# Performance work log

Hardware: AMD Instinct MI355X
Metric: run time of the kernel (lower is better)

Reference implementation:

```python
import jax, jax.numpy as jnp
import numpy as np

DIM = 384
HEADS = 6
NEG = -1e9  # masked-score fill; equivalent to gathering only kept K/V rows


def setup_inputs() -> dict:
    key = jax.random.key(0)
    ks = jax.random.split(key, 9)
    B, N, C = 1, 4098, DIM
    x = jax.random.normal(ks[0], (B, N, C), dtype=jnp.float32)
    pos = jax.random.normal(ks[1], (B, N + 1, C), dtype=jnp.float32)
    # float mask in [0,1); >=0.5 means 'foreground / keep as key', <0.5 pooled into back token
    mask = jax.random.uniform(ks[2], (B, 1, N - 2), dtype=jnp.float32)
    mask_block = jnp.ones((N + 1,), dtype=jnp.float32)  # positions 0, N-1, N always kept
    Wq = jax.random.normal(ks[3], (C, C), dtype=jnp.float32) * 0.02
    Wk = jax.random.normal(ks[4], (C, C), dtype=jnp.float32) * 0.02
    Wv = jax.random.normal(ks[5], (C, C), dtype=jnp.float32) * 0.02
    Wp = jax.random.normal(ks[6], (C, C), dtype=jnp.float32) * 0.02
    bp = jnp.zeros((C,), dtype=jnp.float32)
    return {"x": x, "pos": pos, "mask": mask, "mask_block": mask_block,
            "Wq": Wq, "Wk": Wk, "Wv": Wv, "Wp": Wp, "bp": bp}


def reference(x, pos, mask, mask_block, Wq, Wk, Wv, Wp, bp):
    B, N, C = x.shape
    H = HEADS
    D = C // H
    scale = D ** -0.5
    eps = 1e-10

    # back token: average of background (mask < 0.5) interior tokens
    reverse = jnp.where(mask < 0.5, 1.0, 0.0)                      # (B,1,N-2)
    pooled = jnp.einsum('bon,bnc->boc', reverse, x[:, 1:N - 1])    # (B,1,C)
    back_tokens = pooled / (reverse.sum(axis=2, keepdims=True) + eps)

    kv_x = jnp.concatenate([x, back_tokens], axis=1)               # (B,N+1,C)
    q_x = x + pos[:, :N]
    k_x = kv_x + pos

    q = (q_x @ Wq.T).reshape(B, N, H, D).transpose(0, 2, 1, 3)       # (B,H,N,D)
    k = (k_x @ Wk.T).reshape(B, N + 1, H, D).transpose(0, 2, 1, 3)   # (B,H,N+1,D)
    v = (kv_x @ Wv.T).reshape(B, N + 1, H, D).transpose(0, 2, 1, 3)  # (B,H,N+1,D)

    # key-selection mask: original gathers rows with mask_block >= 0.5;
    # masked softmax over all N+1 keys is mathematically identical.
    mb = mask_block.at[1:N - 1].set(mask[0, 0])
    keep = mb >= 0.5                                               # (N+1,)

    scores = jnp.einsum('bhqd,bhkd->bhqk', q, k) * scale
    scores = jnp.where(keep[None, None, None, :], scores, NEG)
    attn = jax.nn.softmax(scores, axis=-1)
    out = jnp.einsum('bhqk,bhkd->bhqd', attn, v)
    out = out.transpose(0, 2, 1, 3).reshape(B, N, C)
    return out @ Wp.T + bp
```

## Files before the change

kernel.cpp:

```cpp
#include <hip/hip_runtime.h>
#include <math.h>

#define N_TOK 4098
#define NK_TOK 4099
#define C_DIM 384
#define NKPAD 4160

typedef short  bh8 __attribute__((ext_vector_type(8)));
typedef float  f32x4 __attribute__((ext_vector_type(4)));
typedef unsigned short ushort;
typedef ushort u4 __attribute__((ext_vector_type(4)));
typedef ushort u8 __attribute__((ext_vector_type(8)));

static __device__ __forceinline__ ushort f2bf(float f) {
  unsigned int u = __float_as_uint(f);
  u = (u + 0x7FFF + ((u >> 16) & 1)) >> 16;
  return (ushort)u;
}
static __device__ __forceinline__ float bf2f(ushort s) {
  return __uint_as_float(((unsigned int)s) << 16);
}

__global__ __launch_bounds__(256) void prep_kernel(
    const float* __restrict__ x, const float* __restrict__ pos,
    const float* __restrict__ mask, const float* __restrict__ mask_block,
    const float* __restrict__ Wq, const float* __restrict__ Wk,
    const float* __restrict__ Wv, const float* __restrict__ Wp,
    float* __restrict__ pooled_part, float* __restrict__ cnt_part,
    int* __restrict__ nk, int* __restrict__ inv,
    ushort* __restrict__ Ak, ushort* __restrict__ Av, ushort* __restrict__ Wb) {
  const int b = blockIdx.x, t = threadIdx.x;
  if (b < 64) {
    __shared__ float smask[64];
    const int r0 = b * 64;
    if (t < 64) smask[t] = mask[r0 + t];
    __syncthreads();
    float a0 = 0.f, a1 = 0.f;
    int lc = 0;
#pragma unroll 8
    for (int i = 0; i < 64; ++i) {
      if (smask[i] < 0.5f) {
        a0 += x[(size_t)(r0 + i + 1) * C_DIM + t];
        if (t < 128) a1 += x[(size_t)(r0 + i + 1) * C_DIM + 256 + t];
        ++lc;
      }
    }
    pooled_part[b * C_DIM + t] = a0;
    if (t < 128) pooled_part[b * C_DIM + 256 + t] = a1;
    if (t == 0) cnt_part[b] = (float)lc;
  } else if (b == 64) {
    __shared__ int scnt[256];
    const int j0 = t * 17;
    unsigned int bits = 0;
    int c = 0;
#pragma unroll 1
    for (int u = 0; u < 17; ++u) {
      const int j = j0 + u;
      bool keep = false;
      if (j < NK_TOK)
        keep = (j >= 1 && j <= N_TOK - 2) ? (mask[j - 1] >= 0.5f)
                                          : (mask_block[j] >= 0.5f);
      if (keep) { bits |= 1u << u; ++c; }
    }
    scnt[t] = c;
    __syncthreads();
    for (int d = 1; d < 256; d <<= 1) {
      const int v = scnt[t];
      const int add = (t >= d) ? scnt[t - d] : 0;
      __syncthreads();
      scnt[t] = v + add;
      __syncthreads();
    }
    int base = scnt[t] - c;
    if (t == 255) *nk = scnt[255];
#pragma unroll 1
    for (int u = 0; u < 17; ++u) {
      const int j = j0 + u;
      if (j < NK_TOK) inv[j] = ((bits >> u) & 1) ? base++ : -1;
    }
  } else if (b < 194) {
    const int r0 = (b - 65) * 32;
#pragma unroll 3
    for (int i = 0; i < 12; ++i) {
      const int idx = i * 1024 + t * 4;
      const int row = r0 + idx / C_DIM, col = idx % C_DIM;
      if (row >= N_TOK) continue;
      const float4 pv = *(const float4*)&pos[(size_t)row * C_DIM + col];
      const float4 xv = *(const float4*)&x[(size_t)row * C_DIM + col];
      u4 k4 = {f2bf(xv.x + pv.x), f2bf(xv.y + pv.y),
               f2bf(xv.z + pv.z), f2bf(xv.w + pv.w)};
      *(u4*)&Ak[(size_t)row * C_DIM + col] = k4;
      u4 v4 = {f2bf(xv.x), f2bf(xv.y), f2bf(xv.z), f2bf(xv.w)};
      *(u4*)&Av[(size_t)row * C_DIM + col] = v4;
    }
  } else {
    const int wi = b - 194;
    const float* src = (wi < 8) ? Wq : (wi < 16) ? Wk : (wi < 24) ? Wv : Wp;
    const int base = (wi >> 3) * 147456 + (wi & 7) * 18432;
#pragma unroll 2
    for (int i = 0; i < 18; ++i) {
      const float4 v = *(const float4*)&src[(wi & 7) * 18432 + i * 1024 + t * 4];
      u4 o = {f2bf(v.x), f2bf(v.y), f2bf(v.z), f2bf(v.w)};
      *(u4*)&Wb[base + i * 1024 + t * 4] = o;
    }
  }
}

static __device__ __forceinline__ void gemm_core(
    const ushort* __restrict__ A, const ushort* __restrict__ B,
    ushort (* __restrict__ As)[72], ushort (* __restrict__ Bs)[72],
    int t, int w, int quad, int l15, f32x4 acc[4]) {
  const int g = t & 7;
  u8 ra[2], rb[2];
#pragma unroll
  for (int it = 0; it < 2; ++it) {
    const int r = it * 32 + (t >> 3);
    ra[it] = *(const u8*)&A[r * C_DIM + g * 8];
    rb[it] = *(const u8*)&B[r * C_DIM + g * 8];
  }
#pragma unroll 1
  for (int kt = 0; kt < 6; ++kt) {
    __syncthreads();
#pragma unroll
    for (int it = 0; it < 2; ++it) {
      const int r = it * 32 + (t >> 3);
      *(u8*)&As[r][g * 8] = ra[it];
      *(u8*)&Bs[r][g * 8] = rb[it];
    }
    __syncthreads();
    if (kt < 5) {
      const int k0 = (kt + 1) * 64;
#pragma unroll
      for (int it = 0; it < 2; ++it) {
        const int r = it * 32 + (t >> 3);
        ra[it] = *(const u8*)&A[r * C_DIM + k0 + g * 8];
        rb[it] = *(const u8*)&B[r * C_DIM + k0 + g * 8];
      }
    }
    const bh8 b0 = *(const bh8*)&Bs[w * 16 + l15][quad * 8];
    const bh8 b1 = *(const bh8*)&Bs[w * 16 + l15][32 + quad * 8];
#pragma unroll
    for (int mb = 0; mb < 4; ++mb) {
      const bh8 a0 = *(const bh8*)&As[mb * 16 + l15][quad * 8];
      const bh8 a1 = *(const bh8*)&As[mb * 16 + l15][32 + quad * 8];
      acc[mb] = __builtin_amdgcn_mfma_f32_16x16x32_bf16(a0, b0, acc[mb], 0, 0, 0);
      acc[mb] = __builtin_amdgcn_mfma_f32_16x16x32_bf16(a1, b1, acc[mb], 0, 0, 0);
    }
  }
}

__global__ __launch_bounds__(256) void gemm3_kernel(
    const ushort* __restrict__ Ak, const ushort* __restrict__ Av,
    const ushort* __restrict__ Wb, const int* __restrict__ inv,
    const float* __restrict__ pooled_part, const float* __restrict__ cnt_part,
    const float* __restrict__ pos, ushort* __restrict__ Qh,
    ushort* __restrict__ Kc, ushort* __restrict__ Vt) {
  __shared__ ushort As[64][72], Bs[64][72];
  __shared__ float skin[C_DIM], svin[C_DIM];
  const int t = threadIdx.x, w = t >> 6, lane = t & 63;
  const int quad = lane >> 4, l15 = lane & 15;
  const int which = blockIdx.y / 6, h = blockIdx.y % 6;

  if (blockIdx.x == 65) {
    if (blockIdx.y != 0) return;
    float cs = 0.f;
#pragma unroll 8
    for (int i = 0; i < 64; ++i) cs += cnt_part[i];
    const float ic = 1.f / (cs + 1e-10f);
    for (int c = t; c < C_DIM; c += 256) {
      float s = 0.f;
#pragma unroll 8
      for (int p = 0; p < 64; ++p) s += pooled_part[p * C_DIM + c];
      const float back = s * ic;
      skin[c] = bf2f(f2bf(back + pos[(size_t)(NK_TOK - 1) * C_DIM + c]));
      svin[c] = bf2f(f2bf(back));
    }
    __syncthreads();
    const int slot = inv[NK_TOK - 1];
    for (int o = t; o < C_DIM; o += 256) {
      const ushort* wk = Wb + 147456 + (size_t)o * C_DIM;
      const ushort* wv = Wb + 294912 + (size_t)o * C_DIM;
      float ka = 0.f, va = 0.f;
#pragma unroll 4
      for (int c8 = 0; c8 < 48; ++c8) {
        const u8 k8 = *(const u8*)&wk[c8 * 8];
        const u8 v8 = *(const u8*)&wv[c8 * 8];
#pragma unroll
        for (int j = 0; j < 8; ++j) {
          ka += bf2f(k8[j]) * skin[c8 * 8 + j];
          va += bf2f(v8[j]) * svin[c8 * 8 + j];
        }
      }
      const int hh = o >> 6, d = o & 63;
      Kc[((size_t)hh * NKPAD + slot) * 64 + d] = f2bf(ka);
      Vt[((size_t)(hh * 64 + d)) * NKPAD + slot] = f2bf(va);
    }
    return;
  }

  const int m0 = blockIdx.x * 64;
  const ushort* A = (which == 2 ? Av : Ak) + (size_t)m0 * C_DIM;
  const ushort* B = Wb + (size_t)which * 147456 + (size_t)h * 64 * C_DIM;
  f32x4 acc[4];
#pragma unroll
  for (int i = 0; i < 4; ++i) acc[i] = (f32x4){0.f, 0.f, 0.f, 0.f};
  gemm_core(A, B, As, Bs, t, w, quad, l15, acc);
  const int n = w * 16 + l15;
  if (which == 0) {
#pragma unroll
    for (int mb = 0; mb < 4; ++mb)
#pragma unroll
      for (int r = 0; r < 4; ++r) {
        const int m = m0 + mb * 16 + quad * 4 + r;
        if (m < N_TOK)
          Qh[((size_t)h * N_TOK + m) * 64 + n] = f2bf(acc[mb][r] * 0.125f);
      }
  } else if (which == 1) {
#pragma unroll
    for (int mb = 0; mb < 4; ++mb)
#pragma unroll
      for (int r = 0; r < 4; ++r) {
        const int m = m0 + mb * 16 + quad * 4 + r;
        if (m < NK_TOK - 1) {
          const int slot = inv[m];
          if (slot >= 0) Kc[((size_t)h * NKPAD + slot) * 64 + n] = f2bf(acc[mb][r]);
        }
      }
  } else {
#pragma unroll
    for (int mb = 0; mb < 4; ++mb)
#pragma unroll
      for (int r = 0; r < 4; ++r) {
        const int m = m0 + mb * 16 + quad * 4 + r;
        if (m < NK_TOK - 1) {
          const int slot = inv[m];
          if (slot >= 0) Vt[((size_t)(h * 64 + n)) * NKPAD + slot] = f2bf(acc[mb][r]);
        }
      }
  }
}

__global__ __launch_bounds__(256) void attn_kernel(
    const ushort* __restrict__ Qh, const ushort* __restrict__ Kc,
    const ushort* __restrict__ Vt, const int* __restrict__ nkp,
    ushort* __restrict__ Opart, float* __restrict__ Lpart) {
  __shared__ ushort Ks[64][72];
  __shared__ ushort Vs[64][72];
  __shared__ ushort Ps[4][16][72];
  const int t = threadIdx.x, w = t >> 6, lane = t & 63;
  const int quad = lane >> 4, l15 = lane & 15;
  const int h = blockIdx.y, slice = blockIdx.z;
  const int q0 = blockIdx.x * 64;
  const int nk = *nkp, nchunk = (nk + 63) >> 6;
  const int g = t & 7;

  bh8 qf0, qf1;
  {
    int qr = q0 + w * 16 + l15;
    if (qr > N_TOK - 1) qr = N_TOK - 1;
    const ushort* qp = Qh + ((size_t)h * N_TOK + qr) * 64 + quad * 8;
    qf0 = *(const bh8*)qp;
    qf1 = *(const bh8*)(qp + 32);
  }
  f32x4 oacc[4];
#pragma unroll
  for (int i = 0; i < 4; ++i) oacc[i] = (f32x4){0.f, 0.f, 0.f, 0.f};
  float l_r = 0.f;

  const ushort* kb = Kc + (size_t)h * NKPAD * 64;
  const ushort* vb = Vt + (size_t)h * 64 * NKPAD;

  u8 rk[2], rv[2];
  if (slice < nchunk) {
#pragma unroll
    for (int it = 0; it < 2; ++it) {
      const int r = it * 32 + (t >> 3);
      rk[it] = *(const u8*)&kb[(size_t)(slice * 64 + r) * 64 + g * 8];
      rv[it] = *(const u8*)&vb[(size_t)r * NKPAD + slice * 64 + g * 8];
    }
  }
#pragma unroll 1
  for (int kc = slice; kc < nchunk; kc += 3) {
    __syncthreads();
#pragma unroll
    for (int it = 0; it < 2; ++it) {
      const int r = it * 32 + (t >> 3);
      *(u8*)&Ks[r][g * 8] = rk[it];
      *(u8*)&Vs[r][g * 8] = rv[it];
    }
    __syncthreads();
    if (kc + 3 < nchunk) {
#pragma unroll
      for (int it = 0; it < 2; ++it) {
        const int r = it * 32 + (t >> 3);
        rk[it] = *(const u8*)&kb[(size_t)((kc + 3) * 64 + r) * 64 + g * 8];
        rv[it] = *(const u8*)&vb[(size_t)r * NKPAD + (kc + 3) * 64 + g * 8];
      }
    }
    float csum = 0.f;
#pragma unroll
    for (int f = 0; f < 4; ++f) {
      f32x4 s4 = {0.f, 0.f, 0.f, 0.f};
      const bh8 a0 = *(const bh8*)&Ks[f * 16 + l15][quad * 8];
      const bh8 a1 = *(const bh8*)&Ks[f * 16 + l15][32 + quad * 8];
      s4 = __builtin_amdgcn_mfma_f32_16x16x32_bf16(a0, qf0, s4, 0, 0, 0);
      s4 = __builtin_amdgcn_mfma_f32_16x16x32_bf16(a1, qf1, s4, 0, 0, 0);
      const int keyb = kc * 64 + f * 16 + quad * 4;
      u4 pv;
#pragma unroll
      for (int r = 0; r < 4; ++r) {
        const float p = (keyb + r < nk) ? __expf(s4[r]) : 0.f;
        csum += p;
        pv[r] = f2bf(p);
      }
      *(u4*)&Ps[w][l15][f * 16 + quad * 4] = pv;
    }
    csum += __shfl_xor(csum, 16);
    csum += __shfl_xor(csum, 32);
    l_r += csum;

    const bh8 pa0 = *(const bh8*)&Ps[w][l15][quad * 8];
    const bh8 pa1 = *(const bh8*)&Ps[w][l15][32 + quad * 8];
#pragma unroll
    for (int db = 0; db < 4; ++db) {
      const bh8 b0 = *(const bh8*)&Vs[db * 16 + l15][quad * 8];
      const bh8 b1 = *(const bh8*)&Vs[db * 16 + l15][32 + quad * 8];
      oacc[db] = __builtin_amdgcn_mfma_f32_16x16x32_bf16(pa0, b0, oacc[db], 0, 0, 0);
      oacc[db] = __builtin_amdgcn_mfma_f32_16x16x32_bf16(pa1, b1, oacc[db], 0, 0, 0);
    }
  }

  const int sh = slice * 6 + h;
  const int qg = q0 + w * 16;
#pragma unroll
  for (int db = 0; db < 4; ++db)
#pragma unroll
    for (int r = 0; r < 4; ++r) {
      const int q = qg + quad * 4 + r;
      if (q < N_TOK)
        Opart[((size_t)sh * NKPAD + q) * 64 + db * 16 + l15] = f2bf(oacc[db][r]);
    }
  if (quad == 0) {
    const int q = qg + l15;
    if (q < N_TOK) Lpart[sh * NKPAD + q] = l_r;
  }
}

__global__ __launch_bounds__(256) void gemm_out_kernel(
    const ushort* __restrict__ Opart, const float* __restrict__ Lpart,
    const ushort* __restrict__ Wpb, const float* __restrict__ bp,
    float* __restrict__ out) {
  __shared__ ushort As[64][72], Bs[64][72];
  const int t = threadIdx.x, w = t >> 6, lane = t & 63;
  const int quad = lane >> 4, l15 = lane & 15;
  const int m0 = blockIdx.x * 64;
  const int n0 = blockIdx.y * 64;
  const int g8 = t & 7;
  f32x4 acc[4];
#pragma unroll
  for (int i = 0; i < 4; ++i) acc[i] = (f32x4){0.f, 0.f, 0.f, 0.f};

  u8 ra[2], rb[2];
#pragma unroll
  for (int it = 0; it < 2; ++it) {
    const int r = it * 32 + (t >> 3), m = m0 + r;
    float l = 0.f;
#pragma unroll
    for (int s = 0; s < 3; ++s) l += Lpart[(s * 6 + 0) * NKPAD + m];
    const float invl = 1.f / l;
    float o[8] = {0, 0, 0, 0, 0, 0, 0, 0};
#pragma unroll
    for (int s = 0; s < 3; ++s) {
      const u8 v = *(const u8*)&Opart[((size_t)(s * 6 + 0) * NKPAD + m) * 64 + g8 * 8];
#pragma unroll
      for (int j = 0; j < 8; ++j) o[j] += bf2f(v[j]);
    }
#pragma unroll
    for (int j = 0; j < 8; ++j) ra[it][j] = f2bf(o[j] * invl);
    rb[it] = *(const u8*)&Wpb[(size_t)(n0 + r) * C_DIM + g8 * 8];
  }
#pragma unroll 1
  for (int kt = 0; kt < 6; ++kt) {
    __syncthreads();
#pragma unroll
    for (int it = 0; it < 2; ++it) {
      const int r = it * 32 + (t >> 3);
      *(u8*)&As[r][g8 * 8] = ra[it];
      *(u8*)&Bs[r][g8 * 8] = rb[it];
    }
    __syncthreads();
    if (kt < 5) {
      const int kh = kt + 1;
#pragma unroll
      for (int it = 0; it < 2; ++it) {
        const int r = it * 32 + (t >> 3), m = m0 + r;
        float l = 0.f;
#pragma unroll
        for (int s = 0; s < 3; ++s) l += Lpart[(s * 6 + kh) * NKPAD + m];
        const float invl = 1.f / l;
        float o[8] = {0, 0, 0, 0, 0, 0, 0, 0};
#pragma unroll
        for (int s = 0; s < 3; ++s) {
          const u8 v = *(const u8*)&Opart[((size_t)(s * 6 + kh) * NKPAD + m) * 64 + g8 * 8];
#pragma unroll
          for (int j = 0; j < 8; ++j) o[j] += bf2f(v[j]);
        }
#pragma unroll
        for (int j = 0; j < 8; ++j) ra[it][j] = f2bf(o[j] * invl);
        rb[it] = *(const u8*)&Wpb[(size_t)(n0 + r) * C_DIM + kh * 64 + g8 * 8];
      }
    }
    const bh8 b0 = *(const bh8*)&Bs[w * 16 + l15][quad * 8];
    const bh8 b1 = *(const bh8*)&Bs[w * 16 + l15][32 + quad * 8];
#pragma unroll
    for (int mb = 0; mb < 4; ++mb) {
      const bh8 a0 = *(const bh8*)&As[mb * 16 + l15][quad * 8];
      const bh8 a1 = *(const bh8*)&As[mb * 16 + l15][32 + quad * 8];
      acc[mb] = __builtin_amdgcn_mfma_f32_16x16x32_bf16(a0, b0, acc[mb], 0, 0, 0);
      acc[mb] = __builtin_amdgcn_mfma_f32_16x16x32_bf16(a1, b1, acc[mb], 0, 0, 0);
    }
  }
  const int n = w * 16 + l15;
  const float bb = bp[n0 + n];
#pragma unroll
  for (int mb = 0; mb < 4; ++mb)
#pragma unroll
    for (int r = 0; r < 4; ++r) {
      const int m = m0 + mb * 16 + quad * 4 + r;
      if (m < N_TOK) out[(size_t)m * C_DIM + n0 + n] = acc[mb][r] + bb;
    }
}

extern "C" void kernel_launch(void* const* d_in, const int* in_sizes, int n_in,
                              void* d_out, int out_size, void* d_ws, size_t ws_size,
                              hipStream_t stream) {
  const float* x          = (const float*)d_in[0];
  const float* pos        = (const float*)d_in[1];
  const float* mask       = (const float*)d_in[2];
  const float* mask_block = (const float*)d_in[3];
  const float* Wq         = (const float*)d_in[4];
  const float* Wk         = (const float*)d_in[5];
  const float* Wv         = (const float*)d_in[6];
  const float* Wp         = (const float*)d_in[7];
  const float* bp         = (const float*)d_in[8];
  float* out = (float*)d_out;
  char* wsb = (char*)d_ws;

  float*  cnt_part    = (float*)wsb;
  int*    nk          = (int*)(wsb + 512);
  int*    inv         = (int*)(wsb + 1024);
  float*  pooled_part = (float*)(wsb + 20480);
  ushort* Ak          = (ushort*)(wsb + 217088);
  ushort* Av          = (ushort*)(wsb + 3411968);
  ushort* Wb          = (ushort*)(wsb + 6606848);
  ushort* Qh          = (ushort*)(wsb + 7786496);
  ushort* Kc          = (ushort*)(wsb + 10933760);
  ushort* Vt          = (ushort*)(wsb + 14128640);
  ushort* Op          = (ushort*)(wsb + 17323520);
  float*  Lp          = (float*)(wsb + 26908160);

  prep_kernel<<<dim3(226), dim3(256), 0, stream>>>(
      x, pos, mask, mask_block, Wq, Wk, Wv, Wp,
      pooled_part, cnt_part, nk, inv, Ak, Av, Wb);
  gemm3_kernel<<<dim3(66, 18), dim3(256), 0, stream>>>(
      Ak, Av, Wb, inv, pooled_part, cnt_part, pos, Qh, Kc, Vt);
  attn_kernel<<<dim3(65, 6, 3), dim3(256), 0, stream>>>(Qh, Kc, Vt, nk, Op, Lp);
  gemm_out_kernel<<<dim3(65, 6), dim3(256), 0, stream>>>(Op, Lp, Wb + 3 * 147456,
                                                         bp, out);
}
```

Measured before the change: 166.5 us.

## Enlarge QKV projection tiles to 128x128 with direct global-to-LDS swizzled loads

```diff
diff --git a/kernel.cpp b/kernel.cpp
--- a/kernel.cpp
+++ b/kernel.cpp
@@ -19,6 +19,26 @@
 }
 static __device__ __forceinline__ float bf2f(ushort s) {
   return __uint_as_float(((unsigned int)s) << 16);
+}
+
+typedef const __attribute__((address_space(1))) unsigned int* gas_t;
+typedef __attribute__((address_space(3))) unsigned int* las_t;
+static __device__ __forceinline__ void gload16(const void* g, void* l) {
+  __builtin_amdgcn_global_load_lds((gas_t)g, (las_t)l, 16, 0, 0);
+}
+
+static __device__ __forceinline__ void stage128(const ushort* src, int rs,
+                                                ushort* lds, int t) {
+#pragma unroll
+  for (int it = 0; it < 4; ++it) {
+    const int base = it * 256 + (t & 192);
+    const int i = base + (t & 63);
+    const int r = i >> 3, c8 = i & 7;
+    gload16(src + r * rs + ((c8 ^ (r & 7)) << 3), lds + base * 8);
+  }
+}
+static __device__ __forceinline__ bh8 frag(const ushort* lds, int row, int c8) {
+  return *(const bh8*)&lds[(row << 6) + ((c8 ^ (row & 7)) << 3)];
 }
 
 __global__ __launch_bounds__(256) void prep_kernel(
@@ -106,62 +126,18 @@
   }
 }
 
-static __device__ __forceinline__ void gemm_core(
-    const ushort* __restrict__ A, const ushort* __restrict__ B,
-    ushort (* __restrict__ As)[72], ushort (* __restrict__ Bs)[72],
-    int t, int w, int quad, int l15, f32x4 acc[4]) {
-  const int g = t & 7;
-  u8 ra[2], rb[2];
-#pragma unroll
-  for (int it = 0; it < 2; ++it) {
-    const int r = it * 32 + (t >> 3);
-    ra[it] = *(const u8*)&A[r * C_DIM + g * 8];
-    rb[it] = *(const u8*)&B[r * C_DIM + g * 8];
-  }
-#pragma unroll 1
-  for (int kt = 0; kt < 6; ++kt) {
-    __syncthreads();
-#pragma unroll
-    for (int it = 0; it < 2; ++it) {
-      const int r = it * 32 + (t >> 3);
-      *(u8*)&As[r][g * 8] = ra[it];
-      *(u8*)&Bs[r][g * 8] = rb[it];
-    }
-    __syncthreads();
-    if (kt < 5) {
-      const int k0 = (kt + 1) * 64;
-#pragma unroll
-      for (int it = 0; it < 2; ++it) {
-        const int r = it * 32 + (t >> 3);
-        ra[it] = *(const u8*)&A[r * C_DIM + k0 + g * 8];
-        rb[it] = *(const u8*)&B[r * C_DIM + k0 + g * 8];
-      }
-    }
-    const bh8 b0 = *(const bh8*)&Bs[w * 16 + l15][quad * 8];
-    const bh8 b1 = *(const bh8*)&Bs[w * 16 + l15][32 + quad * 8];
-#pragma unroll
-    for (int mb = 0; mb < 4; ++mb) {
-      const bh8 a0 = *(const bh8*)&As[mb * 16 + l15][quad * 8];
-      const bh8 a1 = *(const bh8*)&As[mb * 16 + l15][32 + quad * 8];
-      acc[mb] = __builtin_amdgcn_mfma_f32_16x16x32_bf16(a0, b0, acc[mb], 0, 0, 0);
-      acc[mb] = __builtin_amdgcn_mfma_f32_16x16x32_bf16(a1, b1, acc[mb], 0, 0, 0);
-    }
-  }
-}
-
 __global__ __launch_bounds__(256) void gemm3_kernel(
     const ushort* __restrict__ Ak, const ushort* __restrict__ Av,
     const ushort* __restrict__ Wb, const int* __restrict__ inv,
     const float* __restrict__ pooled_part, const float* __restrict__ cnt_part,
     const float* __restrict__ pos, ushort* __restrict__ Qh,
     ushort* __restrict__ Kc, ushort* __restrict__ Vt) {
-  __shared__ ushort As[64][72], Bs[64][72];
+  __shared__ ushort As[8192], Bs[8192];
   __shared__ float skin[C_DIM], svin[C_DIM];
   const int t = threadIdx.x, w = t >> 6, lane = t & 63;
   const int quad = lane >> 4, l15 = lane & 15;
-  const int which = blockIdx.y / 6, h = blockIdx.y % 6;
-
-  if (blockIdx.x == 65) {
+
+  if (blockIdx.x == 33) {
     if (blockIdx.y != 0) return;
     float cs = 0.f;
 #pragma unroll 8
@@ -198,45 +174,81 @@
     return;
   }
 
-  const int m0 = blockIdx.x * 64;
+  const int which = blockIdx.y / 3, ntile = blockIdx.y % 3;
+  const int m0 = blockIdx.x * 128;
+  const int n0 = ntile * 128;
   const ushort* A = (which == 2 ? Av : Ak) + (size_t)m0 * C_DIM;
-  const ushort* B = Wb + (size_t)which * 147456 + (size_t)h * 64 * C_DIM;
-  f32x4 acc[4];
-#pragma unroll
-  for (int i = 0; i < 4; ++i) acc[i] = (f32x4){0.f, 0.f, 0.f, 0.f};
-  gemm_core(A, B, As, Bs, t, w, quad, l15, acc);
-  const int n = w * 16 + l15;
-  if (which == 0) {
-#pragma unroll
-    for (int mb = 0; mb < 4; ++mb)
-#pragma unroll
-      for (int r = 0; r < 4; ++r) {
-        const int m = m0 + mb * 16 + quad * 4 + r;
-        if (m < N_TOK)
-          Qh[((size_t)h * N_TOK + m) * 64 + n] = f2bf(acc[mb][r] * 0.125f);
-      }
-  } else if (which == 1) {
-#pragma unroll
-    for (int mb = 0; mb < 4; ++mb)
-#pragma unroll
-      for (int r = 0; r < 4; ++r) {
-        const int m = m0 + mb * 16 + quad * 4 + r;
-        if (m < NK_TOK - 1) {
-          const int slot = inv[m];
-          if (slot >= 0) Kc[((size_t)h * NKPAD + slot) * 64 + n] = f2bf(acc[mb][r]);
+  const ushort* B = Wb + (size_t)which * 147456 + (size_t)n0 * C_DIM;
+  const int wr = w >> 1, wc = w & 1;
+
+  f32x4 acc[4][4];
+#pragma unroll
+  for (int i = 0; i < 4; ++i)
+#pragma unroll
+    for (int j = 0; j < 4; ++j) acc[i][j] = (f32x4){0.f, 0.f, 0.f, 0.f};
+
+#pragma unroll 1
+  for (int kt = 0; kt < 6; ++kt) {
+    __syncthreads();
+    stage128(A + kt * 64, C_DIM, As, t);
+    stage128(B + kt * 64, C_DIM, Bs, t);
+    __syncthreads();
+    bh8 bf[4][2];
+#pragma unroll
+    for (int nb = 0; nb < 4; ++nb) {
+      bf[nb][0] = frag(Bs, wc * 64 + nb * 16 + l15, quad);
+      bf[nb][1] = frag(Bs, wc * 64 + nb * 16 + l15, 4 + quad);
+    }
+#pragma unroll
+    for (int mb = 0; mb < 4; ++mb) {
+      const bh8 a0 = frag(As, wr * 64 + mb * 16 + l15, quad);
+      const bh8 a1 = frag(As, wr * 64 + mb * 16 + l15, 4 + quad);
+#pragma unroll
+      for (int nb = 0; nb < 4; ++nb) {
+        acc[mb][nb] = __builtin_amdgcn_mfma_f32_16x16x32_bf16(a0, bf[nb][0], acc[mb][nb], 0, 0, 0);
+        acc[mb][nb] = __builtin_amdgcn_mfma_f32_16x16x32_bf16(a1, bf[nb][1], acc[mb][nb], 0, 0, 0);
+      }
+    }
+  }
+
+#pragma unroll
+  for (int nb = 0; nb < 4; ++nb) {
+    const int col = n0 + wc * 64 + nb * 16 + l15;
+    const int h = col >> 6, d = col & 63;
+    if (which == 0) {
+#pragma unroll
+      for (int mb = 0; mb < 4; ++mb)
+#pragma unroll
+        for (int r = 0; r < 4; ++r) {
+          const int m = m0 + wr * 64 + mb * 16 + quad * 4 + r;
+          if (m < N_TOK)
+            Qh[((size_t)h * N_TOK + m) * 64 + d] = f2bf(acc[mb][nb][r] * 0.125f);
         }
-      }
-  } else {
-#pragma unroll
-    for (int mb = 0; mb < 4; ++mb)
-#pragma unroll
-      for (int r = 0; r < 4; ++r) {
-        const int m = m0 + mb * 16 + quad * 4 + r;
-        if (m < NK_TOK - 1) {
-          const int slot = inv[m];
-          if (slot >= 0) Vt[((size_t)(h * 64 + n)) * NKPAD + slot] = f2bf(acc[mb][r]);
+    } else if (which == 1) {
+#pragma unroll
+      for (int mb = 0; mb < 4; ++mb)
+#pragma unroll
+        for (int r = 0; r < 4; ++r) {
+          const int m = m0 + wr * 64 + mb * 16 + quad * 4 + r;
+          if (m < NK_TOK - 1) {
+            const int slot = inv[m];
+            if (slot >= 0)
+              Kc[((size_t)h * NKPAD + slot) * 64 + d] = f2bf(acc[mb][nb][r]);
+          }
         }
-      }
+    } else {
+#pragma unroll
+      for (int mb = 0; mb < 4; ++mb)
+#pragma unroll
+        for (int r = 0; r < 4; ++r) {
+          const int m = m0 + wr * 64 + mb * 16 + quad * 4 + r;
+          if (m < NK_TOK - 1) {
+            const int slot = inv[m];
+            if (slot >= 0)
+              Vt[((size_t)(h * 64 + d)) * NKPAD + slot] = f2bf(acc[mb][nb][r]);
+          }
+        }
+    }
   }
 }
 
@@ -462,7 +474,7 @@
   prep_kernel<<<dim3(226), dim3(256), 0, stream>>>(
       x, pos, mask, mask_block, Wq, Wk, Wv, Wp,
       pooled_part, cnt_part, nk, inv, Ak, Av, Wb);
-  gemm3_kernel<<<dim3(66, 18), dim3(256), 0, stream>>>(
+  gemm3_kernel<<<dim3(34, 9), dim3(256), 0, stream>>>(
       Ak, Av, Wb, inv, pooled_part, cnt_part, pos, Qh, Kc, Vt);
   attn_kernel<<<dim3(65, 6, 3), dim3(256), 0, stream>>>(Qh, Kc, Vt, nk, Op, Lp);
   gemm_out_kernel<<<dim3(65, 6), dim3(256), 0, stream>>>(Op, Lp, Wb + 3 * 147456,
```

Measured after the change: 170.1 us. 1.02x slower.
